# Performance work log

Hardware: AMD Instinct MI355X
Metric: run time of the kernel (lower is better)

Reference implementation:

```python
import jax, jax.numpy as jnp
import numpy as np

EMBED_DIM = 1024
NUM_HEADS = 16
HEAD_DIM = EMBED_DIM // NUM_HEADS


def setup_inputs() -> dict:
    key = jax.random.key(0)
    ks = jax.random.split(key, 7)
    B, N, C = 2, 2048, EMBED_DIM
    s = 1.0 / np.sqrt(C)
    return {
        "x": jax.random.normal(ks[0], (B, N, C), dtype=jnp.float32),
        "phase_signal": jax.random.uniform(ks[1], (B,), dtype=jnp.float32),
        "qkv_w": jax.random.normal(ks[2], (3 * C, C), dtype=jnp.float32) * s,
        "qkv_b": jnp.zeros((3 * C,), dtype=jnp.float32),
        "proj_w": jax.random.normal(ks[3], (C, C), dtype=jnp.float32) * s,
        "proj_b": jnp.zeros((C,), dtype=jnp.float32),
        "phase_weight": jnp.ones((NUM_HEADS,), dtype=jnp.float32),
    }


def reference(x, phase_signal, qkv_w, qkv_b, proj_w, proj_b, phase_weight):
    B, N, C = x.shape
    H, D = NUM_HEADS, HEAD_DIM
    # qkv projection: [B,N,3C] -> [3,B,H,N,D]
    qkv = (x @ qkv_w.T + qkv_b).reshape(B, N, 3, H, D)
    qkv = jnp.transpose(qkv, (2, 0, 3, 1, 4))
    q, k, v = qkv[0], qkv[1], qkv[2]
    attn = jnp.einsum("bhnd,bhmd->bhnm", q, k) * (D ** -0.5)
    # per-(batch, head) phase modulation applied before softmax
    phase_mod = phase_weight[None, :, None, None] * phase_signal[:, None, None, None]
    attn = attn * (1.0 + 0.2 * phase_mod)
    attn = jax.nn.softmax(attn, axis=-1)  # dropout is identity in eval mode
    out = jnp.einsum("bhnm,bhmd->bhnd", attn, v)
    out = jnp.transpose(out, (0, 2, 1, 3)).reshape(B, N, C)
    return out @ proj_w.T + proj_b
```

## Files before the change

kernel.cpp:

```cpp
#include <hip/hip_runtime.h>
#include <stdint.h>

#define NUM_H 16
#define HD    64
#define CDIM  1024
#define NSEQ  2048
#define NBATCH 2
#define LOG2E 1.4426950408889634f

typedef __attribute__((ext_vector_type(8))) short short8;
typedef __attribute__((ext_vector_type(4))) float f32x4;
typedef __attribute__((ext_vector_type(16))) float f32x16;
typedef __attribute__((ext_vector_type(4))) unsigned short ushort4v;
typedef __attribute__((ext_vector_type(4))) float float4v;
typedef __attribute__((ext_vector_type(2))) unsigned int u32x2;

__device__ __forceinline__ unsigned short f2bf(float f) {
    unsigned int u = __builtin_bit_cast(unsigned int, f);
    unsigned int r = u + 0x7fffu + ((u >> 16) & 1u);
    return (unsigned short)(r >> 16);
}

__device__ __forceinline__ unsigned int cvtpk(float a, float b) {
    unsigned int r;
    asm("v_cvt_pk_bf16_f32 %0, %1, %2" : "=v"(r) : "v"(a), "v"(b));
    return r;
}

__device__ __forceinline__ void plswap(unsigned int &a, unsigned int &b) {
    asm("v_permlane32_swap_b32 %0, %1" : "+v"(a), "+v"(b));
}

__device__ __forceinline__ void gload_lds16(const void* g, const void* l) {
    __builtin_amdgcn_global_load_lds(
        (const __attribute__((address_space(1))) unsigned int*)(unsigned long long)(uintptr_t)g,
        (__attribute__((address_space(3))) unsigned int*)(unsigned int)(uintptr_t)l,
        16, 0, 0);
}

__global__ void cvt_bf16_kernel(const float* __restrict__ in,
                                unsigned short* __restrict__ out, int n4) {
    int i = blockIdx.x * blockDim.x + threadIdx.x;
    if (i < n4) {
        float4v v = *(const float4v*)(in + (size_t)i * 4);
        ushort4v o;
        o[0] = f2bf(v[0]); o[1] = f2bf(v[1]); o[2] = f2bf(v[2]); o[3] = f2bf(v[3]);
        *(ushort4v*)(out + (size_t)i * 4) = o;
    }
}

__global__ __launch_bounds__(512, 2) void gemm_qkv(
    const unsigned short* __restrict__ A,
    const unsigned short* __restrict__ Bw,
    const float* __restrict__ bias,
    const float* __restrict__ ps,
    const float* __restrict__ pw,
    unsigned short* __restrict__ qb,
    unsigned short* __restrict__ kfrag,
    unsigned short* __restrict__ vfrag)
{
    __shared__ unsigned short lds[2][2][2][128][64];

    const int tid = threadIdx.x;
    const int wid = tid >> 6;
    const int lane = tid & 63;
    const int l15 = lane & 15, l4 = lane >> 4;
    const int wave_m = wid >> 2, wave_n = wid & 3;

    const int bm = blockIdx.x;
    const int bn = blockIdx.y;

    f32x4 acc[8][4];
    const f32x4 zero4 = {0.f, 0.f, 0.f, 0.f};
#pragma unroll
    for (int m = 0; m < 8; ++m)
#pragma unroll
        for (int n = 0; n < 4; ++n) acc[m][n] = zero4;

    const int jr = lane >> 3;
    const int jc = ((lane & 7) ^ jr) << 4;
    const char* aB = (const char*)A  + (size_t)(bm * 256) * 2048;
    const char* bB = (const char*)Bw + (size_t)(bn * 256) * 2048;

    auto stageH = [&](int t, int which) {
        const int buf = t & 1;
        const int op = which >> 1, hf = which & 1;
        const char* src = (op == 0) ? aB : bB;
        const int rowb = hf * 128 + wid * 16;
        const size_t k0b = (size_t)t * 128;
        char* dst = (char*)&lds[buf][op][hf][wid * 16][0];
#pragma unroll
        for (int i = 0; i < 2; ++i)
            gload_lds16(src + (size_t)(rowb + i * 8 + jr) * 2048 + k0b + jc,
                        dst + i * 1024);
    };

    const int swz = (l15 & 7) << 4;
    auto rdA = [&](int buf, int mq, int mp, int kk) -> short8 {
        return *(const short8*)((const char*)&lds[buf][0][wave_m][mq * 64 + mp * 16 + l15][0]
                                + ((kk * 64 + l4 * 16) ^ swz));
    };
    auto rdB = [&](int buf, int nq, int np, int kk) -> short8 {
        const int br = wave_n * 64 + nq * 32 + np * 16 + l15;
        return *(const short8*)((const char*)&lds[buf][1][br >> 7][br & 127][0]
                                + ((kk * 64 + l4 * 16) ^ swz));
    };

    stageH(0, 0); stageH(0, 1); stageH(0, 2); stageH(0, 3);
    stageH(1, 2); stageH(1, 3); stageH(1, 0); stageH(1, 1);
    asm volatile("s_waitcnt vmcnt(8)" ::: "memory");
    __builtin_amdgcn_s_barrier();

    for (int t = 0; t < 16; ++t) {
        const int buf = t & 1;
        short8 af[4][2], bf[2][2][2];

#pragma unroll
        for (int mp = 0; mp < 4; ++mp) {
            af[mp][0] = rdA(buf, 0, mp, 0); af[mp][1] = rdA(buf, 0, mp, 1);
        }
#pragma unroll
        for (int np = 0; np < 2; ++np) {
            bf[0][np][0] = rdB(buf, 0, np, 0); bf[0][np][1] = rdB(buf, 0, np, 1);
        }
        __builtin_amdgcn_s_barrier();
        __builtin_amdgcn_s_setprio(1);
#pragma unroll
        for (int mp = 0; mp < 4; ++mp)
#pragma unroll
            for (int np = 0; np < 2; ++np)
#pragma unroll
                for (int kk = 0; kk < 2; ++kk)
                    acc[mp][np] = __builtin_amdgcn_mfma_f32_16x16x32_bf16(
                        af[mp][kk], bf[0][np][kk], acc[mp][np], 0, 0, 0);
        __builtin_amdgcn_s_setprio(0);
        __builtin_amdgcn_s_barrier();

#pragma unroll
        for (int np = 0; np < 2; ++np) {
            bf[1][np][0] = rdB(buf, 1, np, 0); bf[1][np][1] = rdB(buf, 1, np, 1);
        }
        if (t < 14) stageH(t + 2, 2);
        __builtin_amdgcn_s_barrier();
        __builtin_amdgcn_s_setprio(1);
#pragma unroll
        for (int mp = 0; mp < 4; ++mp)
#pragma unroll
            for (int np = 0; np < 2; ++np)
#pragma unroll
                for (int kk = 0; kk < 2; ++kk)
                    acc[mp][2 + np] = __builtin_amdgcn_mfma_f32_16x16x32_bf16(
                        af[mp][kk], bf[1][np][kk], acc[mp][2 + np], 0, 0, 0);
        __builtin_amdgcn_s_setprio(0);
        __builtin_amdgcn_s_barrier();

#pragma unroll
        for (int mp = 0; mp < 4; ++mp) {
            af[mp][0] = rdA(buf, 1, mp, 0); af[mp][1] = rdA(buf, 1, mp, 1);
        }
        if (t < 14) stageH(t + 2, 3);
        __builtin_amdgcn_s_barrier();
        __builtin_amdgcn_s_setprio(1);
#pragma unroll
        for (int mp = 0; mp < 4; ++mp)
#pragma unroll
            for (int np = 0; np < 2; ++np)
#pragma unroll
                for (int kk = 0; kk < 2; ++kk)
                    acc[4 + mp][np] = __builtin_amdgcn_mfma_f32_16x16x32_bf16(
                        af[mp][kk], bf[0][np][kk], acc[4 + mp][np], 0, 0, 0);
        __builtin_amdgcn_s_setprio(0);
        __builtin_amdgcn_s_barrier();

        if (t < 14) { stageH(t + 2, 0); stageH(t + 2, 1); }
        __builtin_amdgcn_s_barrier();
        __builtin_amdgcn_s_setprio(1);
#pragma unroll
        for (int mp = 0; mp < 4; ++mp)
#pragma unroll
            for (int np = 0; np < 2; ++np)
#pragma unroll
                for (int kk = 0; kk < 2; ++kk)
                    acc[4 + mp][2 + np] = __builtin_amdgcn_mfma_f32_16x16x32_bf16(
                        af[mp][kk], bf[1][np][kk], acc[4 + mp][2 + np], 0, 0, 0);
        __builtin_amdgcn_s_setprio(0);
        if (t < 14)       { asm volatile("s_waitcnt vmcnt(8)" ::: "memory"); }
        else if (t == 14) { asm volatile("s_waitcnt vmcnt(0)" ::: "memory"); }
        __builtin_amdgcn_s_barrier();
    }

    const int col_base = bn * 256 + wave_n * 64;
    const int t3b = bn >> 2;
    const int bb = bm >> 3;
    const int nn0 = (bm & 7) * 256;
    char* tbc = (char*)&lds[0][0][0][0][0];

    __syncthreads();

    if (t3b == 0) {
#pragma unroll
        for (int n = 0; n < 4; ++n) {
            const int d = n * 16 + l15;
            const float bv = bias[col_base + n * 16 + l15];
#pragma unroll
            for (int m = 0; m < 8; ++m) {
#pragma unroll
                for (int r = 0; r < 4; ++r) {
                    const int tt = wave_m * 128 + m * 16 + l4 * 4 + r;
                    *(unsigned short*)(tbc + wave_n * 32768 + tt * 128 +
                                       ((d * 2) ^ ((tt & 7) << 4))) = f2bf(acc[m][n][r] + bv);
                }
            }
        }
        __syncthreads();
#pragma unroll
        for (int i = 0; i < 16; ++i) {
            const int hq = i >> 2, sub = i & 3;
            const int tt = sub * 64 + (tid >> 3);
            const int chunk = tid & 7;
            const short8 v = *(const short8*)(tbc + hq * 32768 + tt * 128 +
                                              ((chunk * 16) ^ ((tt & 7) << 4)));
            *(short8*)(qb + ((size_t)(bb * 16 + bn * 4 + hq) * 2048 + nn0 + tt) * 64 + chunk * 8) = v;
        }
    } else if (t3b == 1) {
        const float ps0 = ps[0], ps1 = ps[1];
        const int hh = (bn - 4) * 4 + wave_n;
        const float kf = 0.125f * LOG2E *
                         (1.f + 0.2f * pw[hh] * ((bb == 0) ? ps0 : ps1));
#pragma unroll
        for (int n = 0; n < 4; ++n) {
            const int hi_ = l15 >> 3, e = l15 & 7;
            const float bv = bias[col_base + n * 16 + l15];
#pragma unroll
            for (int m = 0; m < 8; ++m) {
#pragma unroll
                for (int r = 0; r < 4; ++r) {
                    const int tt = wave_m * 128 + m * 16 + l4 * 4 + r;
                    const int ti = tt >> 6, u = tt & 63;
                    const int s_ = u >> 5, l31_ = u & 31;
                    *(unsigned short*)(tbc + (((wave_n * 4 + ti) * 8 + s_ * 4 + n) << 10) +
                                       ((hi_ * 32 + l31_) << 4) + e * 2) =
                        f2bf((acc[m][n][r] + bv) * kf);
                }
            }
        }
        __syncthreads();
#pragma unroll
        for (int i = 0; i < 16; ++i) {
            const int hq = i >> 2, ti = i & 3;
            const short8 v = *(const short8*)(tbc + i * 8192 + tid * 16);
            *(short8*)(kfrag + ((size_t)(bb * 16 + (bn - 4) * 4 + hq) * 32 +
                                ((bm & 7) * 4 + ti)) * 4096 + tid * 8) = v;
        }
    } else {
#pragma unroll
        for (int n = 0; n < 4; ++n) {
            const int d = n * 16 + l15;
            const int dt_ = n >> 1, l31_ = d & 31;
            const float bv = bias[col_base + n * 16 + l15];
#pragma unroll
            for (int m = 0; m < 8; ++m) {
#pragma unroll
                for (int r = 0; r < 4; ++r) {
                    const int tt = wave_m * 128 + m * 16 + l4 * 4 + r;
                    const int ti = tt >> 6, u = tt & 63;
                    const int ks = u >> 4, hi_ = (u >> 3) & 1, e = u & 7;
                    *(unsigned short*)(tbc + (((wave_n * 4 + ti) * 8 + dt_ * 4 + ks) << 10) +
                                       ((hi_ * 32 + l31_) << 4) + e * 2) =
                        f2bf(acc[m][n][r] + bv);
                }
            }
        }
        __syncthreads();
#pragma unroll
        for (int i = 0; i < 16; ++i) {
            const int hq = i >> 2, ti = i & 3;
            const short8 v = *(const short8*)(tbc + i * 8192 + tid * 16);
            *(short8*)(vfrag + ((size_t)(bb * 16 + (bn - 8) * 4 + hq) * 32 +
                                ((bm & 7) * 4 + ti)) * 4096 + tid * 8) = v;
        }
    }
}

__global__ __launch_bounds__(256, 2) void gemm_proj(
    const unsigned short* __restrict__ A,
    const unsigned short* __restrict__ Bw,
    const float* __restrict__ bias,
    float* __restrict__ out)
{
    __shared__ unsigned short As[2][128 * 64];
    __shared__ unsigned short Bs[2][128 * 64];
    const int tid = threadIdx.x;
    const int wid = tid >> 6;
    const int lane = tid & 63;
    const int l15 = lane & 15, l4 = lane >> 4;
    const int bm = blockIdx.x, bn = blockIdx.y;
    const int wr = wid >> 1, wc = wid & 1;

    f32x4 acc[4][4];
    const f32x4 zero4 = {0.f, 0.f, 0.f, 0.f};
#pragma unroll
    for (int m = 0; m < 4; ++m)
#pragma unroll
        for (int n = 0; n < 4; ++n) acc[m][n] = zero4;

    const int jr = lane >> 3;
    const int jc = ((lane & 7) ^ jr) << 4;
    const char* aB = (const char*)A  + (size_t)(bm * 128) * 2048;
    const char* bB = (const char*)Bw + (size_t)(bn * 128) * 2048;

    auto stage = [&](int buf, int k0) {
#pragma unroll
        for (int i = 0; i < 4; ++i) {
            const int rowb = wid * 32 + i * 8;
            gload_lds16(aB + (size_t)(rowb + jr) * 2048 + k0 * 2 + jc,
                        (const char*)&As[buf][0] + rowb * 128);
            gload_lds16(bB + (size_t)(rowb + jr) * 2048 + k0 * 2 + jc,
                        (const char*)&Bs[buf][0] + rowb * 128);
        }
    };

    const int swz = (l15 & 7) << 4;

    stage(0, 0);
    for (int it = 0; it < 16; ++it) {
        const int buf = it & 1;
        __syncthreads();
        if (it < 15) stage(buf ^ 1, (it + 1) * 64);
#pragma unroll
        for (int kk = 0; kk < 2; ++kk) {
            short8 a[4], b[4];
#pragma unroll
            for (int m = 0; m < 4; ++m)
                a[m] = *(const short8*)((const char*)&As[buf][0] +
                        (wr * 64 + m * 16 + l15) * 128 + ((kk * 64 + l4 * 16) ^ swz));
#pragma unroll
            for (int n = 0; n < 4; ++n)
                b[n] = *(const short8*)((const char*)&Bs[buf][0] +
                        (wc * 64 + n * 16 + l15) * 128 + ((kk * 64 + l4 * 16) ^ swz));
            __builtin_amdgcn_s_setprio(1);
#pragma unroll
            for (int m = 0; m < 4; ++m)
#pragma unroll
                for (int n = 0; n < 4; ++n)
                    acc[m][n] = __builtin_amdgcn_mfma_f32_16x16x32_bf16(a[m], b[n], acc[m][n], 0, 0, 0);
            __builtin_amdgcn_s_setprio(0);
        }
    }

    const int row_base = bm * 128 + wr * 64;
    const int col_base = bn * 128 + wc * 64;
#pragma unroll
    for (int n = 0; n < 4; ++n) {
        const int col = col_base + n * 16 + l15;
        const float bv = bias[col];
#pragma unroll
        for (int m = 0; m < 4; ++m) {
#pragma unroll
            for (int r = 0; r < 4; ++r) {
                const int row = row_base + m * 16 + l4 * 4 + r;
                out[(size_t)row * 1024 + col] = acc[m][n][r] + bv;
            }
        }
    }
}

__global__ __launch_bounds__(256, 2) void attn_kernel(
    const unsigned short* __restrict__ qb,
    const unsigned short* __restrict__ kfrag,
    const unsigned short* __restrict__ vfrag,
    unsigned short* __restrict__ aout)
{
    __shared__ unsigned short KVs[2][2][4096];

    const int tid = threadIdx.x;
    const int w = tid >> 6;
    const int l = tid & 63;
    const int l31 = l & 31;
    const int hi = l >> 5;

    const int bid = blockIdx.y * 16 + blockIdx.x;
    const int wg = (bid & 7) * 64 + (bid >> 3);
    const int bh = wg >> 4;
    const int b = bh >> 4, h = bh & 15;
    const int q0 = (wg & 15) * 128 + w * 32;

    const char* qg = (const char*)(qb + (size_t)bh * 2048 * 64);
    const unsigned short* kg = kfrag + (size_t)bh * 32 * 4096;
    const unsigned short* vg = vfrag + (size_t)bh * 32 * 4096;

    short8 qf[4];
#pragma unroll
    for (int t = 0; t < 4; ++t)
        qf[t] = *(const short8*)(qg + (size_t)(q0 + l31) * 128 + t * 32 + hi * 16);

    f32x16 oacc[2];
#pragma unroll
    for (int dt = 0; dt < 2; ++dt)
#pragma unroll
        for (int r = 0; r < 16; ++r) oacc[dt][r] = 0.f;
    float lr = 0.f;

    auto stage = [&](int buf, int T) {
#pragma unroll
        for (int i = 0; i < 2; ++i) {
            const int c = w * 2 + i;
            gload_lds16(kg + (size_t)T * 4096 + c * 512 + l * 8, &KVs[buf][0][c * 512]);
            gload_lds16(vg + (size_t)T * 4096 + c * 512 + l * 8, &KVs[buf][1][c * 512]);
        }
    };

    stage(0, 0);
    __syncthreads();

    for (int it = 0; it < 32; ++it) {
        const int buf = it & 1;
        if (it < 31) stage(buf ^ 1, it + 1);

        const unsigned short* Kb = &KVs[buf][0][0];
        const unsigned short* Vb = &KVs[buf][1][0];

        f32x16 sa[2];
        __builtin_amdgcn_s_setprio(1);
#pragma unroll
        for (int s = 0; s < 2; ++s) {
#pragma unroll
            for (int r = 0; r < 16; ++r) sa[s][r] = 0.f;
#pragma unroll
            for (int t = 0; t < 4; ++t) {
                const short8 kf = *(const short8*)(Kb + (s * 4 + t) * 512 + l * 8);
                sa[s] = __builtin_amdgcn_mfma_f32_32x32x16_bf16(kf, qf[t], sa[s], 0, 0, 0);
            }
        }
        __builtin_amdgcn_s_setprio(0);

#pragma unroll
        for (int s = 0; s < 2; ++s)
#pragma unroll
            for (int r = 0; r < 16; ++r)
                sa[s][r] = __builtin_amdgcn_exp2f(sa[s][r] - 20.0f);

        float ts[16];
#pragma unroll
        for (int r = 0; r < 16; ++r) ts[r] = sa[0][r] + sa[1][r];
#pragma unroll
        for (int d = 8; d >= 1; d >>= 1)
#pragma unroll
            for (int r = 0; r < 8; ++r)
                if (r < d) ts[r] += ts[r + d];
        lr += ts[0] + __shfl_xor(ts[0], 32);

#pragma unroll
        for (int s = 0; s < 2; ++s) {
            unsigned int wv[8];
#pragma unroll
            for (int g = 0; g < 8; ++g)
                wv[g] = cvtpk(sa[s][g * 2], sa[s][g * 2 + 1]);
            plswap(wv[0], wv[2]); plswap(wv[1], wv[3]);
            plswap(wv[4], wv[6]); plswap(wv[5], wv[7]);
            union { unsigned int u[4]; short8 s8; } f0, f1;
            f0.u[0] = wv[0]; f0.u[1] = wv[1]; f0.u[2] = wv[2]; f0.u[3] = wv[3];
            f1.u[0] = wv[4]; f1.u[1] = wv[5]; f1.u[2] = wv[6]; f1.u[3] = wv[7];
            __builtin_amdgcn_s_setprio(1);
#pragma unroll
            for (int dt = 0; dt < 2; ++dt) {
                const short8 v0 = *(const short8*)(Vb + (dt * 4 + s * 2 + 0) * 512 + l * 8);
                oacc[dt] = __builtin_amdgcn_mfma_f32_32x32x16_bf16(v0, f0.s8, oacc[dt], 0, 0, 0);
                const short8 v1 = *(const short8*)(Vb + (dt * 4 + s * 2 + 1) * 512 + l * 8);
                oacc[dt] = __builtin_amdgcn_mfma_f32_32x32x16_bf16(v1, f1.s8, oacc[dt], 0, 0, 0);
            }
            __builtin_amdgcn_s_setprio(0);
        }
        __syncthreads();
    }

    const float inv = 1.0f / lr;
    char* outp = (char*)aout + ((size_t)(b * 2048 + q0 + l31) * 1024 + h * 64) * 2;
#pragma unroll
    for (int dt = 0; dt < 2; ++dt)
#pragma unroll
        for (int rg = 0; rg < 4; ++rg) {
            u32x2 pkd;
            pkd[0] = cvtpk(oacc[dt][rg * 4 + 0] * inv, oacc[dt][rg * 4 + 1] * inv);
            pkd[1] = cvtpk(oacc[dt][rg * 4 + 2] * inv, oacc[dt][rg * 4 + 3] * inv);
            *(u32x2*)(outp + (size_t)(dt * 32 + rg * 8 + hi * 4) * 2) = pkd;
        }
}

extern "C" void kernel_launch(void* const* d_in, const int* in_sizes, int n_in,
                              void* d_out, int out_size, void* d_ws, size_t ws_size,
                              hipStream_t stream) {
    const float* x      = (const float*)d_in[0];
    const float* ps     = (const float*)d_in[1];
    const float* qkv_w  = (const float*)d_in[2];
    const float* qkv_b  = (const float*)d_in[3];
    const float* proj_w = (const float*)d_in[4];
    const float* proj_b = (const float*)d_in[5];
    const float* pw     = (const float*)d_in[6];
    float* out = (float*)d_out;
    char* ws = (char*)d_ws;

    unsigned short* x_bf    = (unsigned short*)(ws);
    unsigned short* w1_bf   = (unsigned short*)(ws + (8u  << 20));
    unsigned short* wp_bf   = (unsigned short*)(ws + (14u << 20));
    unsigned short* qb      = (unsigned short*)(ws + (16u << 20));
    unsigned short* kfrag   = (unsigned short*)(ws + (24u << 20));
    unsigned short* vfrag   = (unsigned short*)(ws + (32u << 20));
    unsigned short* attn_bf = x_bf;

    cvt_bf16_kernel<<<4096, 256, 0, stream>>>(x,      x_bf,  1048576);
    cvt_bf16_kernel<<<3072, 256, 0, stream>>>(qkv_w,  w1_bf, 786432);
    cvt_bf16_kernel<<<1024, 256, 0, stream>>>(proj_w, wp_bf, 262144);

    gemm_qkv<<<dim3(16, 12), 512, 0, stream>>>(x_bf, w1_bf, qkv_b, ps, pw, qb, kfrag, vfrag);
    attn_kernel<<<dim3(16, 32), 256, 0, stream>>>(qb, kfrag, vfrag, attn_bf);
    gemm_proj<<<dim3(32, 8), 256, 0, stream>>>(attn_bf, wp_bf, proj_b, out);
}
```

Measured before the change: 110.1 us.

## Merge conversion launches, triple-buffer attention, MFMA row sums, fewer GEMM barriers

```diff
diff --git a/kernel.cpp b/kernel.cpp
--- a/kernel.cpp
+++ b/kernel.cpp
@@ -38,15 +38,21 @@
         16, 0, 0);
 }
 
-__global__ void cvt_bf16_kernel(const float* __restrict__ in,
-                                unsigned short* __restrict__ out, int n4) {
+__global__ void cvt_all_kernel(const float* __restrict__ x,
+                               const float* __restrict__ w1,
+                               const float* __restrict__ wp,
+                               unsigned short* __restrict__ xo,
+                               unsigned short* __restrict__ w1o,
+                               unsigned short* __restrict__ wpo) {
     int i = blockIdx.x * blockDim.x + threadIdx.x;
-    if (i < n4) {
-        float4v v = *(const float4v*)(in + (size_t)i * 4);
-        ushort4v o;
-        o[0] = f2bf(v[0]); o[1] = f2bf(v[1]); o[2] = f2bf(v[2]); o[3] = f2bf(v[3]);
-        *(ushort4v*)(out + (size_t)i * 4) = o;
-    }
+    const float* in; unsigned short* out;
+    if (i < 1048576)      { in = x;  out = xo; }
+    else if (i < 1835008) { in = w1; out = w1o; i -= 1048576; }
+    else                  { in = wp; out = wpo; i -= 1835008; }
+    float4v v = *(const float4v*)(in + (size_t)i * 4);
+    ushort4v o;
+    o[0] = f2bf(v[0]); o[1] = f2bf(v[1]); o[2] = f2bf(v[2]); o[3] = f2bf(v[3]);
+    *(ushort4v*)(out + (size_t)i * 4) = o;
 }
 
 __global__ __launch_bounds__(512, 2) void gemm_qkv(
@@ -120,9 +126,11 @@
             af[mp][0] = rdA(buf, 0, mp, 0); af[mp][1] = rdA(buf, 0, mp, 1);
         }
 #pragma unroll
-        for (int np = 0; np < 2; ++np) {
-            bf[0][np][0] = rdB(buf, 0, np, 0); bf[0][np][1] = rdB(buf, 0, np, 1);
-        }
+        for (int nq = 0; nq < 2; ++nq)
+#pragma unroll
+            for (int np = 0; np < 2; ++np) {
+                bf[nq][np][0] = rdB(buf, nq, np, 0); bf[nq][np][1] = rdB(buf, nq, np, 1);
+            }
         __builtin_amdgcn_s_barrier();
         __builtin_amdgcn_s_setprio(1);
 #pragma unroll
@@ -133,16 +141,6 @@
                 for (int kk = 0; kk < 2; ++kk)
                     acc[mp][np] = __builtin_amdgcn_mfma_f32_16x16x32_bf16(
                         af[mp][kk], bf[0][np][kk], acc[mp][np], 0, 0, 0);
-        __builtin_amdgcn_s_setprio(0);
-        __builtin_amdgcn_s_barrier();
-
-#pragma unroll
-        for (int np = 0; np < 2; ++np) {
-            bf[1][np][0] = rdB(buf, 1, np, 0); bf[1][np][1] = rdB(buf, 1, np, 1);
-        }
-        if (t < 14) stageH(t + 2, 2);
-        __builtin_amdgcn_s_barrier();
-        __builtin_amdgcn_s_setprio(1);
 #pragma unroll
         for (int mp = 0; mp < 4; ++mp)
 #pragma unroll
@@ -158,8 +156,10 @@
         for (int mp = 0; mp < 4; ++mp) {
             af[mp][0] = rdA(buf, 1, mp, 0); af[mp][1] = rdA(buf, 1, mp, 1);
         }
-        if (t < 14) stageH(t + 2, 3);
+        if (t < 14) { stageH(t + 2, 2); stageH(t + 2, 3); }
+        asm volatile("s_waitcnt lgkmcnt(0)" ::: "memory");
         __builtin_amdgcn_s_barrier();
+        if (t < 14) { stageH(t + 2, 0); stageH(t + 2, 1); }
         __builtin_amdgcn_s_setprio(1);
 #pragma unroll
         for (int mp = 0; mp < 4; ++mp)
@@ -169,12 +169,6 @@
                 for (int kk = 0; kk < 2; ++kk)
                     acc[4 + mp][np] = __builtin_amdgcn_mfma_f32_16x16x32_bf16(
                         af[mp][kk], bf[0][np][kk], acc[4 + mp][np], 0, 0, 0);
-        __builtin_amdgcn_s_setprio(0);
-        __builtin_amdgcn_s_barrier();
-
-        if (t < 14) { stageH(t + 2, 0); stageH(t + 2, 1); }
-        __builtin_amdgcn_s_barrier();
-        __builtin_amdgcn_s_setprio(1);
 #pragma unroll
         for (int mp = 0; mp < 4; ++mp)
 #pragma unroll
@@ -371,7 +365,7 @@
     const unsigned short* __restrict__ vfrag,
     unsigned short* __restrict__ aout)
 {
-    __shared__ unsigned short KVs[2][2][4096];
+    __shared__ unsigned short KVs[3][2][4096];
 
     const int tid = threadIdx.x;
     const int w = tid >> 6;
@@ -394,12 +388,13 @@
     for (int t = 0; t < 4; ++t)
         qf[t] = *(const short8*)(qg + (size_t)(q0 + l31) * 128 + t * 32 + hi * 16);
 
-    f32x16 oacc[2];
-#pragma unroll
-    for (int dt = 0; dt < 2; ++dt)
-#pragma unroll
-        for (int r = 0; r < 16; ++r) oacc[dt][r] = 0.f;
-    float lr = 0.f;
+    short8 ones;
+#pragma unroll
+    for (int j = 0; j < 8; ++j) ones[j] = (short)0x3F80;
+
+    f32x16 oacc[2], lacc;
+#pragma unroll
+    for (int r = 0; r < 16; ++r) { oacc[0][r] = 0.f; oacc[1][r] = 0.f; lacc[r] = 0.f; }
 
     auto stage = [&](int buf, int T) {
 #pragma unroll
@@ -410,12 +405,14 @@
         }
     };
 
-    stage(0, 0);
-    __syncthreads();
-
+    stage(0, 0); stage(1, 1);
+    asm volatile("s_waitcnt vmcnt(4)" ::: "memory");
+    __builtin_amdgcn_s_barrier();
+
+    int buf = 0;
     for (int it = 0; it < 32; ++it) {
-        const int buf = it & 1;
-        if (it < 31) stage(buf ^ 1, it + 1);
+        int nxt2 = buf + 2; if (nxt2 >= 3) nxt2 -= 3;
+        if (it < 30) stage(nxt2, it + 2);
 
         const unsigned short* Kb = &KVs[buf][0][0];
         const unsigned short* Vb = &KVs[buf][1][0];
@@ -439,16 +436,6 @@
 #pragma unroll
             for (int r = 0; r < 16; ++r)
                 sa[s][r] = __builtin_amdgcn_exp2f(sa[s][r] - 20.0f);
-
-        float ts[16];
-#pragma unroll
-        for (int r = 0; r < 16; ++r) ts[r] = sa[0][r] + sa[1][r];
-#pragma unroll
-        for (int d = 8; d >= 1; d >>= 1)
-#pragma unroll
-            for (int r = 0; r < 8; ++r)
-                if (r < d) ts[r] += ts[r + d];
-        lr += ts[0] + __shfl_xor(ts[0], 32);
 
 #pragma unroll
         for (int s = 0; s < 2; ++s) {
@@ -462,6 +449,8 @@
             f0.u[0] = wv[0]; f0.u[1] = wv[1]; f0.u[2] = wv[2]; f0.u[3] = wv[3];
             f1.u[0] = wv[4]; f1.u[1] = wv[5]; f1.u[2] = wv[6]; f1.u[3] = wv[7];
             __builtin_amdgcn_s_setprio(1);
+            lacc = __builtin_amdgcn_mfma_f32_32x32x16_bf16(ones, f0.s8, lacc, 0, 0, 0);
+            lacc = __builtin_amdgcn_mfma_f32_32x32x16_bf16(ones, f1.s8, lacc, 0, 0, 0);
 #pragma unroll
             for (int dt = 0; dt < 2; ++dt) {
                 const short8 v0 = *(const short8*)(Vb + (dt * 4 + s * 2 + 0) * 512 + l * 8);
@@ -471,10 +460,18 @@
             }
             __builtin_amdgcn_s_setprio(0);
         }
-        __syncthreads();
+
+        if (it < 30) {
+            asm volatile("s_waitcnt vmcnt(4) lgkmcnt(0)" ::: "memory");
+            __builtin_amdgcn_s_barrier();
+        } else if (it == 30) {
+            asm volatile("s_waitcnt vmcnt(0) lgkmcnt(0)" ::: "memory");
+            __builtin_amdgcn_s_barrier();
+        }
+        ++buf; if (buf >= 3) buf -= 3;
     }
 
-    const float inv = 1.0f / lr;
+    const float inv = 1.0f / lacc[0];
     char* outp = (char*)aout + ((size_t)(b * 2048 + q0 + l31) * 1024 + h * 64) * 2;
 #pragma unroll
     for (int dt = 0; dt < 2; ++dt)
@@ -508,10 +505,7 @@
     unsigned short* vfrag   = (unsigned short*)(ws + (32u << 20));
     unsigned short* attn_bf = x_bf;
 
-    cvt_bf16_kernel<<<4096, 256, 0, stream>>>(x,      x_bf,  1048576);
-    cvt_bf16_kernel<<<3072, 256, 0, stream>>>(qkv_w,  w1_bf, 786432);
-    cvt_bf16_kernel<<<1024, 256, 0, stream>>>(proj_w, wp_bf, 262144);
-
+    cvt_all_kernel<<<8192, 256, 0, stream>>>(x, qkv_w, proj_w, x_bf, w1_bf, wp_bf);
     gemm_qkv<<<dim3(16, 12), 512, 0, stream>>>(x_bf, w1_bf, qkv_b, ps, pw, qb, kfrag, vfrag);
     attn_kernel<<<dim3(16, 32), 256, 0, stream>>>(qb, kfrag, vfrag, attn_bf);
     gemm_proj<<<dim3(32, 8), 256, 0, stream>>>(attn_bf, wp_bf, proj_b, out);
```

Result: faster. 107.4 us (-2.5%).
